# Performance work log

Hardware: AMD Instinct MI355X
Metric: run time of the kernel (lower is better)

## Reference

```python
import jax, jax.numpy as jnp
import numpy as np

DIM = 256
HEADS = 8
DIM_HEAD = 32
AGENT = 6
WIN = 7


def _relative_position_index(L, Wh, Ww):
    coords = np.stack(np.meshgrid(np.arange(L), np.arange(Wh), np.arange(Ww), indexing='ij'))
    cf = coords.reshape(3, -1)                      # (3, N)
    rel = cf[:, :, None] - cf[:, None, :]           # (3, N, N)
    rel = rel.transpose(1, 2, 0).astype(np.int64)   # (N, N, 3)
    rel[..., 0] += L - 1
    rel[..., 1] += Wh - 1
    rel[..., 2] += Ww - 1
    rel[..., 0] *= (2 * Wh - 1) * (2 * Ww - 1)
    rel[..., 1] *= 2 * Ww - 1
    return rel.sum(-1)                              # (N, N)


def setup_inputs() -> dict:
    key = jax.random.key(0)
    k1, k2, k3, k4, k5 = jax.random.split(key, 5)
    B, X, Y = 2, 8, 8
    x = jax.random.normal(k1, (B, AGENT, X, Y, WIN, WIN, DIM), dtype=jnp.float32)
    mask = jax.random.randint(k2, (B, X, Y, WIN, WIN, 1, AGENT), 0, 2, dtype=jnp.int32)
    w_qkv = jax.random.normal(k3, (3 * DIM, DIM), dtype=jnp.float32) * 0.02
    w_out = jax.random.normal(k4, (DIM, DIM), dtype=jnp.float32) * 0.02
    n_bias = (2 * AGENT - 1) * (2 * WIN - 1) * (2 * WIN - 1)
    bias_table = jax.random.normal(k5, (n_bias, HEADS), dtype=jnp.float32) * 0.02
    return {"x": x, "mask": mask, "w_qkv": w_qkv, "w_out": w_out, "bias_table": bias_table}


def reference(x, mask, w_qkv, w_out, bias_table):
    B, L, X, Y, W1, W2, C = x.shape
    h, dh = HEADS, DIM_HEAD
    N = L * W1 * W2
    scale = dh ** -0.5

    # 'b l x y w1 w2 d -> (b x y) (l w1 w2) d'
    xr = jnp.transpose(x, (0, 2, 3, 1, 4, 5, 6)).reshape(B * X * Y, N, C)

    qkv = jnp.einsum('bnc,ec->bne', xr, w_qkv)      # (Bw, N, 3C)
    q, k, v = jnp.split(qkv, 3, axis=-1)
    def to_heads(t):
        return jnp.transpose(t.reshape(B * X * Y, N, h, dh), (0, 2, 1, 3))
    q, k, v = to_heads(q) * scale, to_heads(k), to_heads(v)

    sim = jnp.einsum('bhid,bhjd->bhij', q, k)       # (Bw, h, N, N)

    rel_idx = jnp.asarray(_relative_position_index(L, W1, W2))
    bias = bias_table[rel_idx]                      # (N, N, h)
    sim = sim + jnp.transpose(bias, (2, 0, 1))[None]

    # 'b x y w1 w2 e l -> (b x y) e (l w1 w2)'
    m = jnp.transpose(mask, (0, 1, 2, 5, 6, 3, 4)).reshape(B * X * Y, 1, N)
    sim = jnp.where(m[:, :, None, :] == 0, jnp.float32(-1e9), sim)

    attn = jax.nn.softmax(sim, axis=-1)
    out = jnp.einsum('bhij,bhjd->bhid', attn, v)    # (Bw, h, N, dh)

    # 'b h (l w1 w2) d -> b l w1 w2 (h d)'
    out = jnp.transpose(out, (0, 2, 1, 3)).reshape(B * X * Y, L, W1, W2, C)
    out = jnp.einsum('blwvc,ec->blwve', out, w_out)

    # '(b x y) l w1 w2 d -> b l x y w1 w2 d'
    out = out.reshape(B, X, Y, L, W1, W2, C)
    return jnp.transpose(out, (0, 3, 1, 2, 4, 5, 6))
```

## Files before the change

### kernel.cpp

```cpp
#include <hip/hip_runtime.h>
#include <hip/hip_bf16.h>

#define DIM 256
#define HEADS 8
#define DH 32
#define AGENT 6
#define WIN 7
#define NTOK 294
#define BWIN 128
#define SCALE 0.17677669529663687f
#define TP 19
#define QSTR 40
#define PSTR 328

typedef __hip_bfloat16 bf16;
typedef __attribute__((ext_vector_type(8))) short s16x8;
typedef __attribute__((ext_vector_type(4))) float f32x4;
typedef __attribute__((ext_vector_type(4))) unsigned int u32x4;

__device__ __forceinline__ float bfv(unsigned short u){ return __uint_as_float(((unsigned int)u) << 16); }
__device__ __forceinline__ unsigned short f2bu(float f){
    bf16 b = __float2bfloat16(f); return *reinterpret_cast<unsigned short*>(&b);
}
__device__ __forceinline__ float rdf(const void* p, size_t idx, int isf32) {
    return isf32 ? ((const float*)p)[idx] : bfv(((const unsigned short*)p)[idx]);
}

__device__ __forceinline__ void gll16(const void* gp, void* lp) {
    __builtin_amdgcn_global_load_lds(
        (const __attribute__((address_space(1))) unsigned int*)gp,
        (__attribute__((address_space(3))) unsigned int*)lp, 16, 0, 0);
}

__global__ void detect_kernel(const unsigned short* __restrict__ xraw, int* __restrict__ flag) {
    __shared__ int s;
    if (threadIdx.x == 0) s = 0;
    __syncthreads();
    int bad = 0;
    for (int i = threadIdx.x; i < 8192; i += 256) {
        float v = bfv(xraw[i]);
        if (!(fabsf(v) <= 1e10f)) bad = 1;
    }
    if (bad) atomicOr(&s, 1);
    __syncthreads();
    if (threadIdx.x == 0) *flag = s;
}

__global__ void prepw_kernel(const void* __restrict__ wq, const void* __restrict__ wo,
                             unsigned short* __restrict__ Wq, unsigned short* __restrict__ Wo,
                             const int* __restrict__ flag) {
    if (!*flag) return;
    int c = blockIdx.x * 256 + threadIdx.x;
    const float* src; unsigned short* dst;
    if (c < 24576) { src = (const float*)wq + c * 8; dst = Wq + (size_t)c * 8; }
    else           { src = (const float*)wo + (size_t)(c - 24576) * 8; dst = Wo + (size_t)(c - 24576) * 8; }
    float4 v0 = ((const float4*)src)[0], v1 = ((const float4*)src)[1];
    s16x8 u;
    u[0] = (short)f2bu(v0.x); u[1] = (short)f2bu(v0.y); u[2] = (short)f2bu(v0.z); u[3] = (short)f2bu(v0.w);
    u[4] = (short)f2bu(v1.x); u[5] = (short)f2bu(v1.y); u[6] = (short)f2bu(v1.z); u[7] = (short)f2bu(v1.w);
    *(s16x8*)dst = u;
}

__global__ void biasb_kernel(const void* __restrict__ bt, unsigned short* __restrict__ biasB,
                             const int* __restrict__ flag) {
    int idx = blockIdx.x * 256 + threadIdx.x;
    const int total = HEADS * TP * TP * 64;
    if (idx >= total) return;
    const int isf32 = *flag;
    int lane = idx & 63; int t = idx >> 6;
    int jt = t % TP; t /= TP; int it = t % TP; int h = t / TP;
    int i = it * 16 + (lane & 15);
    int g = lane >> 4;
    ushort4 v;
    unsigned short* vp = (unsigned short*)&v;
    #pragma unroll
    for (int r = 0; r < 4; r++) {
        int j = jt * 16 + g * 4 + r;
        float val = 0.f;
        if (i < NTOK && j < NTOK) {
            int li = i / 49, ri = i - li * 49, w1i = ri / 7, w2i = ri - w1i * 7;
            int lj = j / 49, rj = j - lj * 49, w1j = rj / 7, w2j = rj - w1j * 7;
            int rel = (li - lj + AGENT - 1) * 169 + (w1i - w1j + WIN - 1) * 13 + (w2i - w2j + WIN - 1);
            val = rdf(bt, (size_t)rel * HEADS + h, isf32);
        }
        vp[r] = f2bu(val);
    }
    ((ushort4*)biasB)[idx] = v;
}

__device__ __forceinline__ void stage64_g(const unsigned short* __restrict__ g,
                                          unsigned short* lds, size_t rowBase) {
    const int lane = threadIdx.x & 63, wv = threadIdx.x >> 6;
    const int sub = lane >> 5;
    const int colB = (lane & 31) << 4;
    #pragma unroll
    for (int k = 0; k < 8; k++) {
        const int rr = (wv * 8 + k) * 2 + sub;
        const int cg = colB ^ ((rr & 7) << 4);
        gll16((const char*)g + (rowBase + (size_t)rr) * 512 + cg,
              lds + (size_t)(wv * 8 + k) * 512);
    }
}

__device__ __forceinline__ void stage64_f(const float* __restrict__ g,
                                          unsigned short* lds, size_t rowBase) {
    const int tid = threadIdx.x;
    #pragma unroll
    for (int k = 0; k < 8; k++) {
        int ch = k * 256 + tid;
        int rr = ch >> 5;
        int cB = (ch & 31) << 4;
        int cg = cB ^ ((rr & 7) << 4);
        const f32x4* s4 = (const f32x4*)(g + (rowBase + (size_t)rr) * 256 + (cg >> 1));
        f32x4 v0 = __builtin_nontemporal_load(s4);
        f32x4 v1 = __builtin_nontemporal_load(s4 + 1);
        s16x8 u;
        u[0] = (short)f2bu(v0[0]); u[1] = (short)f2bu(v0[1]); u[2] = (short)f2bu(v0[2]); u[3] = (short)f2bu(v0[3]);
        u[4] = (short)f2bu(v1[0]); u[5] = (short)f2bu(v1[1]); u[6] = (short)f2bu(v1[2]); u[7] = (short)f2bu(v1[3]);
        *(s16x8*)(lds + (size_t)rr * 256 + (cB >> 1)) = u;
    }
}

__global__ __launch_bounds__(256) void qkv_mfma(
    const void* __restrict__ xin, const void* __restrict__ wraw,
    const unsigned short* __restrict__ Wq,
    bf16* __restrict__ Q, bf16* __restrict__ K, bf16* __restrict__ V,
    const int* __restrict__ flag) {
    __shared__ unsigned short As[64 * 256];
    __shared__ unsigned short Bs[64 * 256];
    const int isf32 = *flag;
    const size_t mBase = (size_t)blockIdx.x * 64;
    const unsigned short* Wsrc = isf32 ? Wq : (const unsigned short*)wraw;
    if (isf32) stage64_f((const float*)xin, As, mBase);
    else       stage64_g((const unsigned short*)xin, As, mBase);
    const int tid = threadIdx.x;
    const int wave = tid >> 6, lane = tid & 63;
    const int li = lane & 15, g = lane >> 4;
    const int wm = wave & 1, wn = wave >> 1;
    unsigned int rowOff[2][4];
    #pragma unroll
    for (int mi = 0; mi < 2; mi++)
        #pragma unroll
        for (int r = 0; r < 4; r++) {
            unsigned int m = (unsigned int)mBase + wm * 32 + mi * 16 + g * 4 + r;
            unsigned int w2 = m % 7u, t1 = m / 7u;
            unsigned int w1 = t1 % 7u, t2 = t1 / 7u;
            unsigned int yy = t2 & 7u, t3 = t2 >> 3;
            unsigned int xx = t3 & 7u, t4 = t3 >> 3;
            unsigned int l = t4 % 6u, b = t4 / 6u;
            unsigned int bw = (b << 6) | (xx << 3) | yy;
            unsigned int n = l * 49u + w1 * 7u + w2;
            rowOff[mi][r] = bw * 75264u + n * 32u;
        }
    const int koX = (li & 7) * 8;
    for (int pc = 0; pc < 12; pc++) {
        __syncthreads();
        stage64_g(Wsrc, Bs, (size_t)pc * 64);
        __syncthreads();
        f32x4 acc[2][2];
        #pragma unroll
        for (int mi = 0; mi < 2; mi++)
            #pragma unroll
            for (int ni = 0; ni < 2; ni++) acc[mi][ni] = (f32x4){0.f, 0.f, 0.f, 0.f};
        #pragma unroll
        for (int kc = 0; kc < 8; kc++) {
            const int ko = (kc * 32 + g * 8) ^ koX;
            s16x8 a0 = *(const s16x8*)&As[(wm * 32 + li) * 256 + ko];
            s16x8 a1 = *(const s16x8*)&As[(wm * 32 + 16 + li) * 256 + ko];
            s16x8 b0 = *(const s16x8*)&Bs[(wn * 32 + li) * 256 + ko];
            s16x8 b1 = *(const s16x8*)&Bs[(wn * 32 + 16 + li) * 256 + ko];
            acc[0][0] = __builtin_amdgcn_mfma_f32_16x16x32_bf16(a0, b0, acc[0][0], 0, 0, 0);
            acc[0][1] = __builtin_amdgcn_mfma_f32_16x16x32_bf16(a0, b1, acc[0][1], 0, 0, 0);
            acc[1][0] = __builtin_amdgcn_mfma_f32_16x16x32_bf16(a1, b0, acc[1][0], 0, 0, 0);
            acc[1][1] = __builtin_amdgcn_mfma_f32_16x16x32_bf16(a1, b1, acc[1][1], 0, 0, 0);
        }
        const int p = pc >> 2;
        bf16* dst = (p == 0) ? Q : (p == 1) ? K : V;
        const float sc = (p == 0) ? SCALE : 1.0f;
        const unsigned int hoff = ((pc & 3) * 2 + wn) * 9408u;
        #pragma unroll
        for (int ni = 0; ni < 2; ni++) {
            const unsigned int d = ni * 16 + li;
            #pragma unroll
            for (int mi = 0; mi < 2; mi++)
                #pragma unroll
                for (int r = 0; r < 4; r++)
                    dst[(size_t)(rowOff[mi][r] + hoff + d)] =
                        __float2bfloat16(acc[mi][ni][r] * sc);
        }
    }
}

__global__ __launch_bounds__(512, 2) void attn_mfma(
    const bf16* __restrict__ Q, const bf16* __restrict__ K, const bf16* __restrict__ V,
    const unsigned short* __restrict__ biasB, const int* __restrict__ mask,
    bf16* __restrict__ AT) {
    __shared__ unsigned short Qs[304 * QSTR];
    __shared__ unsigned short Ks[304 * QSTR];
    __shared__ unsigned short Vt[32 * PSTR];
    __shared__ int ms[320];
    const int tid = threadIdx.x;
    const int bw = blockIdx.x >> 3, h = blockIdx.x & 7;
    const size_t base = ((size_t)bw * HEADS + h) * NTOK * DH;
    const unsigned int* Qg = (const unsigned int*)(Q + base);
    const unsigned int* Kg = (const unsigned int*)(K + base);
    const unsigned int* Vg = (const unsigned int*)(V + base);
    for (int gg = tid; gg < NTOK * DH / 2; gg += 512) {
        int r = gg >> 4, d2 = (gg & 15) * 2;
        unsigned int uq = __builtin_nontemporal_load(&Qg[gg]);
        unsigned int uk = __builtin_nontemporal_load(&Kg[gg]);
        unsigned int uv = __builtin_nontemporal_load(&Vg[gg]);
        *(unsigned int*)&Qs[r * QSTR + d2] = uq;
        *(unsigned int*)&Ks[r * QSTR + d2] = uk;
        Vt[d2 * PSTR + r]       = (unsigned short)(uv & 0xffffu);
        Vt[(d2 + 1) * PSTR + r] = (unsigned short)(uv >> 16);
    }
    for (int e = NTOK * QSTR + tid; e < 304 * QSTR; e += 512) { Qs[e] = 0; Ks[e] = 0; }
    for (int idx = tid; idx < 32 * (PSTR - NTOK); idx += 512) {
        int d = idx / (PSTR - NTOK), c = NTOK + idx % (PSTR - NTOK);
        Vt[d * PSTR + c] = 0;
    }
    for (int j = tid; j < 320; j += 512) {
        int mv = 0;
        if (j < NTOK) { int a = j / 49, jr = j - a * 49; mv = mask[((size_t)bw * 49 + jr) * AGENT + a]; }
        ms[j] = mv;
    }
    __syncthreads();
    const int wave = tid >> 6, lane = tid & 63;
    const int li = lane & 15, g = lane >> 4;
    unsigned int mb0 = 0, mb1 = 0, mb2 = 0;
    for (int jt = 0; jt < TP; jt++)
        for (int r = 0; r < 4; r++) {
            int j = jt * 16 + g * 4 + r;
            if (j < NTOK && ms[j]) {
                int bit = jt * 4 + r;
                if (bit < 32) mb0 |= (1u << bit);
                else if (bit < 64) mb1 |= (1u << (bit - 32));
                else mb2 |= (1u << (bit - 64));
            }
        }
    const ushort4* bb = (const ushort4*)biasB + (size_t)h * TP * TP * 64;
    const int sAg = li + ((lane & 16) << 1);
    const int sBg = sAg + 16;
    const bool hiSel = (lane >= 32);
    for (int it = wave; it < TP; it += 8) {
        const s16x8 bq = *(const s16x8*)&Qs[(it * 16 + li) * QSTR + g * 8];
        f32x4 s[TP];
        __builtin_amdgcn_s_setprio(1);
        #pragma unroll
        for (int jt = 0; jt < TP; jt++) {
            ushort4 bv = bb[(it * TP + jt) * 64 + lane];
            f32x4 c = {bfv(bv.x), bfv(bv.y), bfv(bv.z), bfv(bv.w)};
            s16x8 ak = *(const s16x8*)&Ks[(jt * 16 + li) * QSTR + g * 8];
            s[jt] = __builtin_amdgcn_mfma_f32_16x16x32_bf16(ak, bq, c, 0, 0, 0);
        }
        __builtin_amdgcn_s_setprio(0);
        float mx = -INFINITY;
        #pragma unroll
        for (int jt = 0; jt < TP; jt++)
            #pragma unroll
            for (int r = 0; r < 4; r++) {
                int bit = jt * 4 + r;
                unsigned int w = (bit < 32) ? mb0 : (bit < 64) ? mb1 : mb2;
                float sv = ((w >> (bit & 31)) & 1u) ? s[jt][r] : -1e9f;
                if (jt == TP - 1 && g * 4 + r >= 6) sv = -INFINITY;
                s[jt][r] = sv;
                mx = fmaxf(mx, sv);
            }
        mx = fmaxf(mx, __shfl_xor(mx, 16));
        mx = fmaxf(mx, __shfl_xor(mx, 32));
        float sum = 0.f;
        unsigned int p0[TP], p1[TP];
        #pragma unroll
        for (int jt = 0; jt < TP; jt++) {
            float e0 = __expf(s[jt][0] - mx);
            float e1 = __expf(s[jt][1] - mx);
            float e2 = __expf(s[jt][2] - mx);
            float e3 = __expf(s[jt][3] - mx);
            sum += (e0 + e1) + (e2 + e3);
            unsigned int lo, hi;
            asm("v_cvt_pk_bf16_f32 %0, %1, %2" : "=v"(lo) : "v"(e0), "v"(e1));
            asm("v_cvt_pk_bf16_f32 %0, %1, %2" : "=v"(hi) : "v"(e2), "v"(e3));
            p0[jt] = lo; p1[jt] = hi;
        }
        sum += __shfl_xor(sum, 16);
        sum += __shfl_xor(sum, 32);
        const float inv = 1.0f / sum;
        f32x4 o0 = {0.f, 0.f, 0.f, 0.f}, o1 = {0.f, 0.f, 0.f, 0.f};
        #pragma unroll
        for (int kc = 0; kc < 10; kc++) {
            unsigned int a0q = __shfl(p0[2 * kc], sAg);
            unsigned int b0q = __shfl(p1[2 * kc], sAg);
            unsigned int c0q = __shfl(p0[2 * kc], sBg);
            unsigned int d0q = __shfl(p1[2 * kc], sBg);
            unsigned int a1q = 0, b1q = 0, c1q = 0, d1q = 0;
            if (2 * kc + 1 < TP) {
                a1q = __shfl(p0[2 * kc + 1], sAg);
                b1q = __shfl(p1[2 * kc + 1], sAg);
                c1q = __shfl(p0[2 * kc + 1], sBg);
                d1q = __shfl(p1[2 * kc + 1], sBg);
            }
            u32x4 w;
            w[0] = hiSel ? a1q : a0q;
            w[1] = hiSel ? b1q : b0q;
            w[2] = hiSel ? c1q : c0q;
            w[3] = hiSel ? d1q : d0q;
            s16x8 ap = __builtin_bit_cast(s16x8, w);
            s16x8 b0 = *(const s16x8*)&Vt[li * PSTR + kc * 32 + g * 8];
            s16x8 b1 = *(const s16x8*)&Vt[(li + 16) * PSTR + kc * 32 + g * 8];
            __builtin_amdgcn_s_setprio(1);
            o0 = __builtin_amdgcn_mfma_f32_16x16x32_bf16(ap, b0, o0, 0, 0, 0);
            o1 = __builtin_amdgcn_mfma_f32_16x16x32_bf16(ap, b1, o1, 0, 0, 0);
            __builtin_amdgcn_s_setprio(0);
        }
        #pragma unroll
        for (int r = 0; r < 4; r++) {
            float iv = __shfl(inv, g * 4 + r);
            int i = it * 16 + g * 4 + r;
            if (i < NTOK) {
                size_t ob = ((size_t)bw * NTOK + i) * DIM + h * DH;
                AT[ob + li]      = __float2bfloat16(o0[r] * iv);
                AT[ob + 16 + li] = __float2bfloat16(o1[r] * iv);
            }
        }
    }
}

__global__ __launch_bounds__(256) void proj_mfma(
    const bf16* __restrict__ AT, const void* __restrict__ wraw,
    const unsigned short* __restrict__ Wo,
    float* __restrict__ out, const int* __restrict__ flag) {
    __shared__ unsigned short As[64 * 256];
    __shared__ unsigned short Bs[64 * 256];
    const int isf32 = *flag;
    const size_t mBase = (size_t)blockIdx.x * 64;
    const unsigned short* Wsrc = isf32 ? Wo : (const unsigned short*)wraw;
    stage64_g((const unsigned short*)AT, As, mBase);
    const int tid = threadIdx.x;
    const int wave = tid >> 6, lane = tid & 63;
    const int li = lane & 15, g = lane >> 4;
    const int wm = wave & 1, wn = wave >> 1;
    unsigned int offO[2][4];
    #pragma unroll
    for (int mi = 0; mi < 2; mi++)
        #pragma unroll
        for (int r = 0; r < 4; r++) {
            unsigned int m = (unsigned int)mBase + wm * 32 + mi * 16 + g * 4 + r;
            unsigned int bw = m / 294u, n = m - bw * 294u;
            unsigned int b = bw >> 6, xx = (bw >> 3) & 7u, yy = bw & 7u;
            unsigned int l = n / 49u, rr = n - l * 49u, w1 = rr / 7u, w2 = rr - w1 * 7u;
            offO[mi][r] = ((((((b * 6u + l) * 8u + xx) * 8u + yy) * 7u + w1) * 7u) + w2) * 256u;
        }
    const int koX = (li & 7) * 8;
    for (int ec = 0; ec < 4; ec++) {
        __syncthreads();
        stage64_g(Wsrc, Bs, (size_t)ec * 64);
        __syncthreads();
        f32x4 acc[2][2];
        #pragma unroll
        for (int mi = 0; mi < 2; mi++)
            #pragma unroll
            for (int ni = 0; ni < 2; ni++) acc[mi][ni] = (f32x4){0.f, 0.f, 0.f, 0.f};
        #pragma unroll
        for (int kc = 0; kc < 8; kc++) {
            const int ko = (kc * 32 + g * 8) ^ koX;
            s16x8 a0 = *(const s16x8*)&As[(wm * 32 + li) * 256 + ko];
            s16x8 a1 = *(const s16x8*)&As[(wm * 32 + 16 + li) * 256 + ko];
            s16x8 b0 = *(const s16x8*)&Bs[(wn * 32 + li) * 256 + ko];
            s16x8 b1 = *(const s16x8*)&Bs[(wn * 32 + 16 + li) * 256 + ko];
            acc[0][0] = __builtin_amdgcn_mfma_f32_16x16x32_bf16(a0, b0, acc[0][0], 0, 0, 0);
            acc[0][1] = __builtin_amdgcn_mfma_f32_16x16x32_bf16(a0, b1, acc[0][1], 0, 0, 0);
            acc[1][0] = __builtin_amdgcn_mfma_f32_16x16x32_bf16(a1, b0, acc[1][0], 0, 0, 0);
            acc[1][1] = __builtin_amdgcn_mfma_f32_16x16x32_bf16(a1, b1, acc[1][1], 0, 0, 0);
        }
        #pragma unroll
        for (int ni = 0; ni < 2; ni++) {
            const unsigned int e = ec * 64 + wn * 32 + ni * 16 + li;
            #pragma unroll
            for (int mi = 0; mi < 2; mi++)
                #pragma unroll
                for (int r = 0; r < 4; r++)
                    __builtin_nontemporal_store(acc[mi][ni][r],
                        &out[(size_t)(offO[mi][r] + e)]);
        }
    }
}

extern "C" void kernel_launch(void* const* d_in, const int* in_sizes, int n_in,
                              void* d_out, int out_size, void* d_ws, size_t ws_size,
                              hipStream_t stream) {
    const long long SZ_X = 9633792, SZ_M = 37632, SZ_WQ = 196608, SZ_WO = 65536, SZ_BT = 14872;
    const void* x = d_in[0]; const void* maskp = d_in[1]; const void* wqkv = d_in[2];
    const void* wout = d_in[3]; const void* btab = d_in[4];
    for (int i = 0; i < n_in; i++) {
        long long s = in_sizes[i];
        if (s == SZ_X) x = d_in[i];
        else if (s == SZ_M) maskp = d_in[i];
        else if (s == SZ_WQ) wqkv = d_in[i];
        else if (s == SZ_WO) wout = d_in[i];
        else if (s == SZ_BT) btab = d_in[i];
    }
    const int* mask = (const int*)maskp;
    float* out = (float*)d_out;
    const size_t SZ = (size_t)BWIN * NTOK * DIM;
    bf16* Q  = (bf16*)d_ws;
    bf16* K  = Q + SZ;
    bf16* V  = K + SZ;
    bf16* AT = V + SZ;
    unsigned short* biasB = (unsigned short*)(AT + SZ);
    const size_t NBB = (size_t)HEADS * TP * TP * 64 * 4;
    unsigned short* Wq = biasB + NBB;
    unsigned short* Wo = Wq + 196608;
    int* flag = (int*)(Wo + 65536);
    detect_kernel<<<dim3(1), dim3(256), 0, stream>>>((const unsigned short*)x, flag);
    prepw_kernel<<<dim3(128), dim3(256), 0, stream>>>(wqkv, wout, Wq, Wo, flag);
    biasb_kernel<<<dim3((HEADS * TP * TP * 64 + 255) / 256), dim3(256), 0, stream>>>(btab, biasB, flag);
    qkv_mfma<<<dim3(588), dim3(256), 0, stream>>>(x, wqkv, Wq, Q, K, V, flag);
    attn_mfma<<<dim3(BWIN * HEADS), dim3(512), 0, stream>>>(Q, K, V, biasB, mask, AT);
    proj_mfma<<<dim3(588), dim3(256), 0, stream>>>(AT, wout, Wo, out, flag);
}
```

Baseline: 213.8 us.

## Merge prep kernels, use exp2 softmax, and swizzle transposed V in LDS

Three small setup kernels (dtype detection, weight conversion, bias tile build) become one prep kernel that runs detection in every block. qkv repeats the detection itself, which removes two launches and the flag round-trip. Softmax now uses exp2 with log2e folded into the Q scale and the bias table, replacing expf. The transposed V tile in LDS gets a smaller stride plus an XOR swizzle to cut bank conflicts. The cost is a redundant detection pass in every prep and qkv block, plus an extra weight copy when inputs are already bf16.

```diff
diff --git a/kernel.cpp b/kernel.cpp
--- a/kernel.cpp
+++ b/kernel.cpp
@@ -9,21 +9,32 @@
 #define NTOK 294
 #define BWIN 128
 #define SCALE 0.17677669529663687f
+#define LOG2E 1.4426950408889634f
 #define TP 19
 #define QSTR 40
-#define PSTR 328
+#define PSTR 320
 
 typedef __hip_bfloat16 bf16;
 typedef __attribute__((ext_vector_type(8))) short s16x8;
 typedef __attribute__((ext_vector_type(4))) float f32x4;
 typedef __attribute__((ext_vector_type(4))) unsigned int u32x4;
 
+#if __has_builtin(__builtin_amdgcn_exp2f)
+#define EXP2(x) __builtin_amdgcn_exp2f(x)
+#else
+#define EXP2(x) exp2f(x)
+#endif
+
 __device__ __forceinline__ float bfv(unsigned short u){ return __uint_as_float(((unsigned int)u) << 16); }
 __device__ __forceinline__ unsigned short f2bu(float f){
     bf16 b = __float2bfloat16(f); return *reinterpret_cast<unsigned short*>(&b);
 }
 __device__ __forceinline__ float rdf(const void* p, size_t idx, int isf32) {
     return isf32 ? ((const float*)p)[idx] : bfv(((const unsigned short*)p)[idx]);
+}
+
+__device__ __forceinline__ int vtswz(int d, int cByte) {
+    return (d * (PSTR * 2) + cByte) ^ (((d >> 1) & 7) << 4);
 }
 
 __device__ __forceinline__ void gll16(const void* gp, void* lp) {
@@ -32,60 +43,65 @@
         (__attribute__((address_space(3))) unsigned int*)lp, 16, 0, 0);
 }
 
-__global__ void detect_kernel(const unsigned short* __restrict__ xraw, int* __restrict__ flag) {
-    __shared__ int s;
-    if (threadIdx.x == 0) s = 0;
+__device__ __forceinline__ int detect_flag(const unsigned short* __restrict__ xraw,
+                                           int* sflag, int nthreads) {
+    if (threadIdx.x == 0) *sflag = 0;
     __syncthreads();
     int bad = 0;
-    for (int i = threadIdx.x; i < 8192; i += 256) {
+    for (int i = threadIdx.x; i < 8192; i += nthreads) {
         float v = bfv(xraw[i]);
         if (!(fabsf(v) <= 1e10f)) bad = 1;
     }
-    if (bad) atomicOr(&s, 1);
+    if (bad) atomicOr(sflag, 1);
     __syncthreads();
-    if (threadIdx.x == 0) *flag = s;
-}
-
-__global__ void prepw_kernel(const void* __restrict__ wq, const void* __restrict__ wo,
-                             unsigned short* __restrict__ Wq, unsigned short* __restrict__ Wo,
-                             const int* __restrict__ flag) {
-    if (!*flag) return;
-    int c = blockIdx.x * 256 + threadIdx.x;
-    const float* src; unsigned short* dst;
-    if (c < 24576) { src = (const float*)wq + c * 8; dst = Wq + (size_t)c * 8; }
-    else           { src = (const float*)wo + (size_t)(c - 24576) * 8; dst = Wo + (size_t)(c - 24576) * 8; }
-    float4 v0 = ((const float4*)src)[0], v1 = ((const float4*)src)[1];
-    s16x8 u;
-    u[0] = (short)f2bu(v0.x); u[1] = (short)f2bu(v0.y); u[2] = (short)f2bu(v0.z); u[3] = (short)f2bu(v0.w);
-    u[4] = (short)f2bu(v1.x); u[5] = (short)f2bu(v1.y); u[6] = (short)f2bu(v1.z); u[7] = (short)f2bu(v1.w);
-    *(s16x8*)dst = u;
-}
-
-__global__ void biasb_kernel(const void* __restrict__ bt, unsigned short* __restrict__ biasB,
-                             const int* __restrict__ flag) {
-    int idx = blockIdx.x * 256 + threadIdx.x;
-    const int total = HEADS * TP * TP * 64;
-    if (idx >= total) return;
-    const int isf32 = *flag;
-    int lane = idx & 63; int t = idx >> 6;
-    int jt = t % TP; t /= TP; int it = t % TP; int h = t / TP;
-    int i = it * 16 + (lane & 15);
-    int g = lane >> 4;
-    ushort4 v;
-    unsigned short* vp = (unsigned short*)&v;
-    #pragma unroll
-    for (int r = 0; r < 4; r++) {
-        int j = jt * 16 + g * 4 + r;
-        float val = 0.f;
-        if (i < NTOK && j < NTOK) {
-            int li = i / 49, ri = i - li * 49, w1i = ri / 7, w2i = ri - w1i * 7;
-            int lj = j / 49, rj = j - lj * 49, w1j = rj / 7, w2j = rj - w1j * 7;
-            int rel = (li - lj + AGENT - 1) * 169 + (w1i - w1j + WIN - 1) * 13 + (w2i - w2j + WIN - 1);
-            val = rdf(bt, (size_t)rel * HEADS + h, isf32);
-        }
-        vp[r] = f2bu(val);
-    }
-    ((ushort4*)biasB)[idx] = v;
+    return *sflag;
+}
+
+__global__ __launch_bounds__(256) void prep_kernel(
+    const unsigned short* __restrict__ xraw,
+    const void* __restrict__ wq, const void* __restrict__ wo, const void* __restrict__ bt,
+    unsigned short* __restrict__ Wq, unsigned short* __restrict__ Wo,
+    unsigned short* __restrict__ biasB) {
+    __shared__ int sflag;
+    const int isf32 = detect_flag(xraw, &sflag, 256);
+    const int bid = blockIdx.x;
+    if (bid < 722) {
+        int idx = bid * 256 + threadIdx.x;
+        int lane = idx & 63; int t = idx >> 6;
+        int jt = t % TP; t /= TP; int it = t % TP; int h = t / TP;
+        int i = it * 16 + (lane & 15);
+        int g = lane >> 4;
+        ushort4 v;
+        unsigned short* vp = (unsigned short*)&v;
+        #pragma unroll
+        for (int r = 0; r < 4; r++) {
+            int j = jt * 16 + g * 4 + r;
+            float val = 0.f;
+            if (i < NTOK && j < NTOK) {
+                int li = i / 49, ri = i - li * 49, w1i = ri / 7, w2i = ri - w1i * 7;
+                int lj = j / 49, rj = j - lj * 49, w1j = rj / 7, w2j = rj - w1j * 7;
+                int rel = (li - lj + AGENT - 1) * 169 + (w1i - w1j + WIN - 1) * 13 + (w2i - w2j + WIN - 1);
+                val = rdf(bt, (size_t)rel * HEADS + h, isf32) * LOG2E;
+            }
+            vp[r] = f2bu(val);
+        }
+        ((ushort4*)biasB)[idx] = v;
+    } else {
+        int c = (bid - 722) * 256 + threadIdx.x;
+        const void* src; unsigned short* dst; size_t off;
+        if (c < 24576) { src = wq; dst = Wq; off = (size_t)c * 8; }
+        else           { src = wo; dst = Wo; off = (size_t)(c - 24576) * 8; }
+        if (isf32) {
+            const float4* s4 = (const float4*)((const float*)src + off);
+            float4 v0 = s4[0], v1 = s4[1];
+            s16x8 u;
+            u[0] = (short)f2bu(v0.x); u[1] = (short)f2bu(v0.y); u[2] = (short)f2bu(v0.z); u[3] = (short)f2bu(v0.w);
+            u[4] = (short)f2bu(v1.x); u[5] = (short)f2bu(v1.y); u[6] = (short)f2bu(v1.z); u[7] = (short)f2bu(v1.w);
+            *(s16x8*)(dst + off) = u;
+        } else {
+            *(uint4*)(dst + off) = *(const uint4*)((const unsigned short*)src + off);
+        }
+    }
 }
 
 __device__ __forceinline__ void stage64_g(const unsigned short* __restrict__ g,
@@ -122,15 +138,13 @@
 }
 
 __global__ __launch_bounds__(256) void qkv_mfma(
-    const void* __restrict__ xin, const void* __restrict__ wraw,
-    const unsigned short* __restrict__ Wq,
-    bf16* __restrict__ Q, bf16* __restrict__ K, bf16* __restrict__ V,
-    const int* __restrict__ flag) {
+    const void* __restrict__ xin, const unsigned short* __restrict__ Wq,
+    bf16* __restrict__ Q, bf16* __restrict__ K, bf16* __restrict__ V) {
     __shared__ unsigned short As[64 * 256];
     __shared__ unsigned short Bs[64 * 256];
-    const int isf32 = *flag;
+    __shared__ int sflag;
+    const int isf32 = detect_flag((const unsigned short*)xin, &sflag, 256);
     const size_t mBase = (size_t)blockIdx.x * 64;
-    const unsigned short* Wsrc = isf32 ? Wq : (const unsigned short*)wraw;
     if (isf32) stage64_f((const float*)xin, As, mBase);
     else       stage64_g((const unsigned short*)xin, As, mBase);
     const int tid = threadIdx.x;
@@ -155,7 +169,7 @@
     const int koX = (li & 7) * 8;
     for (int pc = 0; pc < 12; pc++) {
         __syncthreads();
-        stage64_g(Wsrc, Bs, (size_t)pc * 64);
+        stage64_g(Wq, Bs, (size_t)pc * 64);
         __syncthreads();
         f32x4 acc[2][2];
         #pragma unroll
@@ -176,7 +190,7 @@
         }
         const int p = pc >> 2;
         bf16* dst = (p == 0) ? Q : (p == 1) ? K : V;
-        const float sc = (p == 0) ? SCALE : 1.0f;
+        const float sc = (p == 0) ? (SCALE * LOG2E) : 1.0f;
         const unsigned int hoff = ((pc & 3) * 2 + wn) * 9408u;
         #pragma unroll
         for (int ni = 0; ni < 2; ni++) {
@@ -205,6 +219,7 @@
     const unsigned int* Qg = (const unsigned int*)(Q + base);
     const unsigned int* Kg = (const unsigned int*)(K + base);
     const unsigned int* Vg = (const unsigned int*)(V + base);
+    char* VtB = (char*)Vt;
     for (int gg = tid; gg < NTOK * DH / 2; gg += 512) {
         int r = gg >> 4, d2 = (gg & 15) * 2;
         unsigned int uq = __builtin_nontemporal_load(&Qg[gg]);
@@ -212,13 +227,13 @@
         unsigned int uv = __builtin_nontemporal_load(&Vg[gg]);
         *(unsigned int*)&Qs[r * QSTR + d2] = uq;
         *(unsigned int*)&Ks[r * QSTR + d2] = uk;
-        Vt[d2 * PSTR + r]       = (unsigned short)(uv & 0xffffu);
-        Vt[(d2 + 1) * PSTR + r] = (unsigned short)(uv >> 16);
+        *(unsigned short*)(VtB + vtswz(d2,     r * 2)) = (unsigned short)(uv & 0xffffu);
+        *(unsigned short*)(VtB + vtswz(d2 + 1, r * 2)) = (unsigned short)(uv >> 16);
     }
     for (int e = NTOK * QSTR + tid; e < 304 * QSTR; e += 512) { Qs[e] = 0; Ks[e] = 0; }
     for (int idx = tid; idx < 32 * (PSTR - NTOK); idx += 512) {
         int d = idx / (PSTR - NTOK), c = NTOK + idx % (PSTR - NTOK);
-        Vt[d * PSTR + c] = 0;
+        *(unsigned short*)(VtB + vtswz(d, c * 2)) = 0;
     }
     for (int j = tid; j < 320; j += 512) {
         int mv = 0;
@@ -273,10 +288,10 @@
         unsigned int p0[TP], p1[TP];
         #pragma unroll
         for (int jt = 0; jt < TP; jt++) {
-            float e0 = __expf(s[jt][0] - mx);
-            float e1 = __expf(s[jt][1] - mx);
-            float e2 = __expf(s[jt][2] - mx);
-            float e3 = __expf(s[jt][3] - mx);
+            float e0 = EXP2(s[jt][0] - mx);
+            float e1 = EXP2(s[jt][1] - mx);
+            float e2 = EXP2(s[jt][2] - mx);
+            float e3 = EXP2(s[jt][3] - mx);
             sum += (e0 + e1) + (e2 + e3);
             unsigned int lo, hi;
             asm("v_cvt_pk_bf16_f32 %0, %1, %2" : "=v"(lo) : "v"(e0), "v"(e1));
@@ -306,8 +321,8 @@
             w[2] = hiSel ? c1q : c0q;
             w[3] = hiSel ? d1q : d0q;
             s16x8 ap = __builtin_bit_cast(s16x8, w);
-            s16x8 b0 = *(const s16x8*)&Vt[li * PSTR + kc * 32 + g * 8];
-            s16x8 b1 = *(const s16x8*)&Vt[(li + 16) * PSTR + kc * 32 + g * 8];
+            s16x8 b0 = *(const s16x8*)(VtB + vtswz(li,      (kc * 32 + g * 8) * 2));
+            s16x8 b1 = *(const s16x8*)(VtB + vtswz(li + 16, (kc * 32 + g * 8) * 2));
             __builtin_amdgcn_s_setprio(1);
             o0 = __builtin_amdgcn_mfma_f32_16x16x32_bf16(ap, b0, o0, 0, 0, 0);
             o1 = __builtin_amdgcn_mfma_f32_16x16x32_bf16(ap, b1, o1, 0, 0, 0);
@@ -327,14 +342,11 @@
 }
 
 __global__ __launch_bounds__(256) void proj_mfma(
-    const bf16* __restrict__ AT, const void* __restrict__ wraw,
-    const unsigned short* __restrict__ Wo,
-    float* __restrict__ out, const int* __restrict__ flag) {
+    const bf16* __restrict__ AT, const unsigned short* __restrict__ Wo,
+    float* __restrict__ out) {
     __shared__ unsigned short As[64 * 256];
     __shared__ unsigned short Bs[64 * 256];
-    const int isf32 = *flag;
     const size_t mBase = (size_t)blockIdx.x * 64;
-    const unsigned short* Wsrc = isf32 ? Wo : (const unsigned short*)wraw;
     stage64_g((const unsigned short*)AT, As, mBase);
     const int tid = threadIdx.x;
     const int wave = tid >> 6, lane = tid & 63;
@@ -354,7 +366,7 @@
     const int koX = (li & 7) * 8;
     for (int ec = 0; ec < 4; ec++) {
         __syncthreads();
-        stage64_g(Wsrc, Bs, (size_t)ec * 64);
+        stage64_g(Wo, Bs, (size_t)ec * 64);
         __syncthreads();
         f32x4 acc[2][2];
         #pragma unroll
@@ -411,11 +423,9 @@
     const size_t NBB = (size_t)HEADS * TP * TP * 64 * 4;
     unsigned short* Wq = biasB + NBB;
     unsigned short* Wo = Wq + 196608;
-    int* flag = (int*)(Wo + 65536);
-    detect_kernel<<<dim3(1), dim3(256), 0, stream>>>((const unsigned short*)x, flag);
-    prepw_kernel<<<dim3(128), dim3(256), 0, stream>>>(wqkv, wout, Wq, Wo, flag);
-    biasb_kernel<<<dim3((HEADS * TP * TP * 64 + 255) / 256), dim3(256), 0, stream>>>(btab, biasB, flag);
-    qkv_mfma<<<dim3(588), dim3(256), 0, stream>>>(x, wqkv, Wq, Q, K, V, flag);
+    prep_kernel<<<dim3(850), dim3(256), 0, stream>>>(
+        (const unsigned short*)x, wqkv, wout, btab, Wq, Wo, biasB);
+    qkv_mfma<<<dim3(588), dim3(256), 0, stream>>>(x, Wq, Q, K, V);
     attn_mfma<<<dim3(BWIN * HEADS), dim3(512), 0, stream>>>(Q, K, V, biasB, mask, AT);
-    proj_mfma<<<dim3(588), dim3(256), 0, stream>>>(AT, wout, Wo, out, flag);
-}
+    proj_mfma<<<dim3(588), dim3(256), 0, stream>>>(AT, Wo, out);
+}
```

Result: no change. 214.6 us (+0.4%).
